# Kernel tuning notes

Measured on AMD Instinct MI355X. Metric: run time of the kernel, lower is better.

Reference implementation:

```python
import jax, jax.numpy as jnp
import numpy as np

U, I, D = 100000, 100000, 64
B, T = 16384, 1_638_400
R = 5  # rating levels 1..5


def setup_inputs() -> dict:
    key = jax.random.key(0)
    ks = jax.random.split(key, 8)
    return {
        "user_idx": jax.random.randint(ks[0], (B,), 0, U, dtype=jnp.int32),
        "item_idx": jax.random.randint(ks[1], (B,), 0, I, dtype=jnp.int32),
        "flat_items": jax.random.randint(ks[2], (T,), 0, I, dtype=jnp.int32),
        "seg_ids": jnp.sort(jax.random.randint(ks[3], (T,), 0, B * R, dtype=jnp.int32)),
        "user_emb": (jax.random.uniform(ks[4], (U, D), dtype=jnp.float32) - 0.5) * 0.01,
        "item_emb": (jax.random.uniform(ks[5], (I, D), dtype=jnp.float32) - 0.5) * 0.01,
        "Mr": (jax.random.uniform(ks[6], (I, D), dtype=jnp.float32) - 0.5) * 0.01,
        "user_bias": jnp.zeros((U,), dtype=jnp.float32),
        "item_bias": jnp.zeros((I,), dtype=jnp.float32),
        "global_avg": jnp.float32(3.5),
    }


def reference(user_idx, item_idx, flat_items, seg_ids, user_emb, item_emb, Mr, user_bias, item_bias, global_avg):
    num_seg = B * R  # segment = sample_i * 5 + (rating - 1)
    # Original torch code does Mr_ik(rate_dict).sum() -> scalar over ALL dims,
    # then broadcasts that scalar onto the latent_dim vector UuMpc[i].
    row_sum = Mr[flat_items].sum(axis=-1)  # [T] per-item full-row sum
    # Emulate `rate_dict.remove(item_idx[i])`: mask out the target item of this sample.
    match = flat_items == item_idx[seg_ids // R]  # [T]
    contrib = jnp.where(match, 0.0, row_sum)
    seg_sum = jax.ops.segment_sum(contrib, seg_ids, num_segments=num_seg)  # [B*5]
    cnt = jax.ops.segment_sum(jnp.where(match, 0.0, 1.0), seg_ids, num_segments=num_seg)
    per_seg = jnp.where(cnt > 0, seg_sum / jnp.sqrt(jnp.maximum(cnt, 1.0)), 0.0)
    uu_mpc = per_seg.reshape(B, R).sum(axis=-1)  # [B] scalar per sample
    user_vec = user_emb[user_idx] + uu_mpc[:, None]  # broadcast scalar over latent dim
    item_vec = item_emb[item_idx]
    rui = (user_vec * item_vec).sum(axis=-1) + user_bias[user_idx] + item_bias[item_idx] + global_avg
    return jnp.clip(rui, 1.0, 5.0)
```

## Files before the change

### kernel.cpp

```cpp
#include <hip/hip_runtime.h>

#define U_N 100000
#define I_N 100000
#define D_N 64
#define B_N 16384
#define T_N 1638400
#define R_N 5
#define NSEG (B_N * R_N)

#define RS_THREADS (I_N * 16)
#define BD_THREADS (T_N / 4)
#define K1_THREADS (RS_THREADS + BD_THREADS)

__global__ void prep_kernel(const float* __restrict__ Mr,
                            const int* __restrict__ seg_ids,
                            float* __restrict__ rowsum,
                            int* __restrict__ seg_start) {
    int gtid = blockIdx.x * blockDim.x + threadIdx.x;
    if (gtid < RS_THREADS) {
        int row = gtid >> 4;
        int sub = gtid & 15;
        const float4* p = (const float4*)(Mr + (long)row * D_N);
        float4 v4 = p[sub];
        float v = v4.x + v4.y + v4.z + v4.w;
        v += __shfl_xor(v, 1);
        v += __shfl_xor(v, 2);
        v += __shfl_xor(v, 4);
        v += __shfl_xor(v, 8);
        if (sub == 0) rowsum[row] = v;
    } else {
        int t4 = gtid - RS_THREADS;
        if (t4 >= BD_THREADS) return;
        int base = t4 * 4;
        int4 s4 = ((const int4*)seg_ids)[t4];
        int sv0 = (base == 0) ? -1 : seg_ids[base - 1];
        int sv1 = s4.x, sv2 = s4.y, sv3 = s4.z, sv4 = s4.w;
        for (int s = sv0 + 1; s <= sv1; ++s) seg_start[s] = base + 0;
        for (int s = sv1 + 1; s <= sv2; ++s) seg_start[s] = base + 1;
        for (int s = sv2 + 1; s <= sv3; ++s) seg_start[s] = base + 2;
        for (int s = sv3 + 1; s <= sv4; ++s) seg_start[s] = base + 3;
        if (base + 4 == T_N) {
            for (int s = sv4 + 1; s <= NSEG; ++s) seg_start[s] = T_N;
        }
    }
}

__device__ __forceinline__ void count_matches(unsigned long long m, int tb,
                                              int e0, int e1, int e2, int e3,
                                              int e4, int e5, int* mcnt) {
    if (m) {
        int ea[6] = {e0, e1, e2, e3, e4, e5};
        #pragma unroll
        for (int r = 0; r < 5; ++r) {
            int a = ea[r] - tb;     a = a < 0 ? 0 : (a > 64 ? 64 : a);
            int bb = ea[r + 1] - tb; bb = bb < 0 ? 0 : (bb > 64 ? 64 : bb);
            if (bb > a) {
                unsigned long long hiM = (bb == 64) ? ~0ULL : ((1ULL << bb) - 1ULL);
                unsigned long long loM = (1ULL << a) - 1ULL;
                mcnt[r] += __popcll(m & hiM & ~loM);
            }
        }
    }
}

__global__ void sample_kernel(const int* __restrict__ user_idx,
                              const int* __restrict__ item_idx,
                              const int* __restrict__ flat_items,
                              const float* __restrict__ user_emb,
                              const float* __restrict__ item_emb,
                              const float* __restrict__ user_bias,
                              const float* __restrict__ item_bias,
                              const float* __restrict__ global_avg,
                              const float* __restrict__ rowsum,
                              const int* __restrict__ seg_start,
                              float* __restrict__ out) {
    int lane = threadIdx.x & 63;
    int b    = (blockIdx.x * blockDim.x + threadIdx.x) >> 6;
    if (b >= B_N) return;

    int u      = user_idx[b];
    int target = item_idx[b];
    float ue = user_emb[(long)u * D_N + lane];
    float ie = item_emb[(long)target * D_N + lane];

    int e0 = seg_start[b * R_N + 0];
    int e1 = seg_start[b * R_N + 1];
    int e2 = seg_start[b * R_N + 2];
    int e3 = seg_start[b * R_N + 3];
    int e4 = seg_start[b * R_N + 4];
    int e5 = seg_start[b * R_N + 5];
    int lo = e0, hi = e5;

    int t0 = lo + lane, t1 = lo + 64 + lane;
    bool ok0 = t0 < hi, ok1 = t1 < hi;
    int fi0 = -1, fi1 = -1;
    float rv0 = 0.f, rv1 = 0.f;
    if (ok0) fi0 = flat_items[t0];
    if (ok1) fi1 = flat_items[t1];
    if (ok0) rv0 = rowsum[fi0];
    if (ok1) rv1 = rowsum[fi1];

    int mcnt[5] = {0, 0, 0, 0, 0};
    unsigned long long m0 = __ballot(ok0 && fi0 == target);
    unsigned long long m1 = __ballot(ok1 && fi1 == target);
    count_matches(m0, lo,      e0, e1, e2, e3, e4, e5, mcnt);
    count_matches(m1, lo + 64, e0, e1, e2, e3, e4, e5, mcnt);
    for (int tb = lo + 128; tb < hi; tb += 64) {
        int t = tb + lane;
        bool ok = t < hi;
        int fi = ok ? flat_items[t] : -1;
        unsigned long long m = __ballot(ok && fi == target);
        count_matches(m, tb, e0, e1, e2, e3, e4, e5, mcnt);
    }

    int c0 = (e1 - e0) - mcnt[0];
    int c1 = (e2 - e1) - mcnt[1];
    int c2 = (e3 - e2) - mcnt[2];
    int c3 = (e4 - e3) - mcnt[3];
    int c4 = (e5 - e4) - mcnt[4];
    float w0 = c0 > 0 ? rsqrtf((float)c0) : 0.f;
    float w1 = c1 > 0 ? rsqrtf((float)c1) : 0.f;
    float w2 = c2 > 0 ? rsqrtf((float)c2) : 0.f;
    float w3 = c3 > 0 ? rsqrtf((float)c3) : 0.f;
    float w4 = c4 > 0 ? rsqrtf((float)c4) : 0.f;

    float acc = 0.f;
    if (ok0 && fi0 != target) {
        float w = t0 >= e1 ? (t0 >= e2 ? (t0 >= e3 ? (t0 >= e4 ? w4 : w3) : w2) : w1) : w0;
        acc += rv0 * w;
    }
    if (ok1 && fi1 != target) {
        float w = t1 >= e1 ? (t1 >= e2 ? (t1 >= e3 ? (t1 >= e4 ? w4 : w3) : w2) : w1) : w0;
        acc += rv1 * w;
    }
    for (int tb = lo + 128; tb < hi; tb += 64) {
        int t = tb + lane;
        if (t < hi) {
            int fi = flat_items[t];
            if (fi != target) {
                float rv = rowsum[fi];
                float w = t >= e1 ? (t >= e2 ? (t >= e3 ? (t >= e4 ? w4 : w3) : w2) : w1) : w0;
                acc += rv * w;
            }
        }
    }

    float dot = ue * ie;
    float isum = ie;
    #pragma unroll
    for (int off = 32; off >= 1; off >>= 1) {
        acc  += __shfl_xor(acc, off);
        dot  += __shfl_xor(dot, off);
        isum += __shfl_xor(isum, off);
    }
    if (lane == 0) {
        float rui = dot + acc * isum + user_bias[u] + item_bias[target] + global_avg[0];
        rui = fminf(fmaxf(rui, 1.0f), 5.0f);
        out[b] = rui;
    }
}

extern "C" void kernel_launch(void* const* d_in, const int* in_sizes, int n_in,
                              void* d_out, int out_size, void* d_ws, size_t ws_size,
                              hipStream_t stream) {
    const int*   user_idx   = (const int*)d_in[0];
    const int*   item_idx   = (const int*)d_in[1];
    const int*   flat_items = (const int*)d_in[2];
    const int*   seg_ids    = (const int*)d_in[3];
    const float* user_emb   = (const float*)d_in[4];
    const float* item_emb   = (const float*)d_in[5];
    const float* Mr         = (const float*)d_in[6];
    const float* user_bias  = (const float*)d_in[7];
    const float* item_bias  = (const float*)d_in[8];
    const float* global_avg = (const float*)d_in[9];
    float* out = (float*)d_out;

    float* rowsum    = (float*)d_ws;
    int*   seg_start = (int*)(rowsum + I_N);

    prep_kernel<<<(K1_THREADS + 255) / 256, 256, 0, stream>>>(
        Mr, seg_ids, rowsum, seg_start);
    sample_kernel<<<B_N / 4, 256, 0, stream>>>(
        user_idx, item_idx, flat_items, user_emb, item_emb,
        user_bias, item_bias, global_avg, rowsum, seg_start, out);
}
```

Baseline: 136.8 us.

## Move embedding dot products into prep kernel and vectorize first segment chunk

The user/item embedding gathers, dot product, item-sum and bias terms move from the sample kernel into extra threads of the prep kernel, which stores a float2 per sample. The sample kernel then handles only the rating-history scan. Its first 256 entries are loaded as one int4 per lane, with per-rating match counts computed by ballots, and later tiles use a simpler ballot-based rating bucket. The intent is to take the embedding latency off the scan kernel and overlap it with the row-sum work. The cost is a larger prep kernel and an extra workspace round trip.

Result: slower. 140.9 us (+3.0%).

```diff
diff --git a/kernel.cpp b/kernel.cpp
--- a/kernel.cpp
+++ b/kernel.cpp
@@ -10,12 +10,21 @@
 
 #define RS_THREADS (I_N * 16)
 #define BD_THREADS (T_N / 4)
-#define K1_THREADS (RS_THREADS + BD_THREADS)
+#define DOT_THREADS (B_N * 64)
+#define K1_THREADS (RS_THREADS + BD_THREADS + DOT_THREADS)
 
 __global__ void prep_kernel(const float* __restrict__ Mr,
                             const int* __restrict__ seg_ids,
+                            const int* __restrict__ user_idx,
+                            const int* __restrict__ item_idx,
+                            const float* __restrict__ user_emb,
+                            const float* __restrict__ item_emb,
+                            const float* __restrict__ user_bias,
+                            const float* __restrict__ item_bias,
+                            const float* __restrict__ global_avg,
                             float* __restrict__ rowsum,
-                            int* __restrict__ seg_start) {
+                            int* __restrict__ seg_start,
+                            float2* __restrict__ pre_isum) {
     int gtid = blockIdx.x * blockDim.x + threadIdx.x;
     if (gtid < RS_THREADS) {
         int row = gtid >> 4;
@@ -28,9 +37,8 @@
         v += __shfl_xor(v, 4);
         v += __shfl_xor(v, 8);
         if (sub == 0) rowsum[row] = v;
-    } else {
+    } else if (gtid < RS_THREADS + BD_THREADS) {
         int t4 = gtid - RS_THREADS;
-        if (t4 >= BD_THREADS) return;
         int base = t4 * 4;
         int4 s4 = ((const int4*)seg_ids)[t4];
         int sv0 = (base == 0) ? -1 : seg_ids[base - 1];
@@ -42,46 +50,45 @@
         if (base + 4 == T_N) {
             for (int s = sv4 + 1; s <= NSEG; ++s) seg_start[s] = T_N;
         }
+    } else {
+        int gt2  = gtid - (RS_THREADS + BD_THREADS);
+        int b    = gt2 >> 6;
+        int lane = gt2 & 63;
+        int u      = user_idx[b];
+        int target = item_idx[b];
+        float ue = user_emb[(long)u * D_N + lane];
+        float ie = item_emb[(long)target * D_N + lane];
+        float ub = user_bias[u];
+        float ib = item_bias[target];
+        float g  = global_avg[0];
+        float dot = ue * ie;
+        float isum = ie;
+        #pragma unroll
+        for (int off = 32; off >= 1; off >>= 1) {
+            dot  += __shfl_xor(dot, off);
+            isum += __shfl_xor(isum, off);
+        }
+        if (lane == 0) {
+            float2 r;
+            r.x = dot + ub + ib + g;
+            r.y = isum;
+            pre_isum[b] = r;
+        }
     }
 }
 
-__device__ __forceinline__ void count_matches(unsigned long long m, int tb,
-                                              int e0, int e1, int e2, int e3,
-                                              int e4, int e5, int* mcnt) {
-    if (m) {
-        int ea[6] = {e0, e1, e2, e3, e4, e5};
-        #pragma unroll
-        for (int r = 0; r < 5; ++r) {
-            int a = ea[r] - tb;     a = a < 0 ? 0 : (a > 64 ? 64 : a);
-            int bb = ea[r + 1] - tb; bb = bb < 0 ? 0 : (bb > 64 ? 64 : bb);
-            if (bb > a) {
-                unsigned long long hiM = (bb == 64) ? ~0ULL : ((1ULL << bb) - 1ULL);
-                unsigned long long loM = (1ULL << a) - 1ULL;
-                mcnt[r] += __popcll(m & hiM & ~loM);
-            }
-        }
-    }
-}
-
-__global__ void sample_kernel(const int* __restrict__ user_idx,
-                              const int* __restrict__ item_idx,
+__global__ void sample_kernel(const int* __restrict__ item_idx,
                               const int* __restrict__ flat_items,
-                              const float* __restrict__ user_emb,
-                              const float* __restrict__ item_emb,
-                              const float* __restrict__ user_bias,
-                              const float* __restrict__ item_bias,
-                              const float* __restrict__ global_avg,
                               const float* __restrict__ rowsum,
                               const int* __restrict__ seg_start,
+                              const float2* __restrict__ pre_isum,
                               float* __restrict__ out) {
     int lane = threadIdx.x & 63;
     int b    = (blockIdx.x * blockDim.x + threadIdx.x) >> 6;
     if (b >= B_N) return;
 
-    int u      = user_idx[b];
     int target = item_idx[b];
-    float ue = user_emb[(long)u * D_N + lane];
-    float ie = item_emb[(long)target * D_N + lane];
+    float2 pi  = pre_isum[b];
 
     int e0 = seg_start[b * R_N + 0];
     int e1 = seg_start[b * R_N + 1];
@@ -91,26 +98,50 @@
     int e5 = seg_start[b * R_N + 5];
     int lo = e0, hi = e5;
 
-    int t0 = lo + lane, t1 = lo + 64 + lane;
-    bool ok0 = t0 < hi, ok1 = t1 < hi;
-    int fi0 = -1, fi1 = -1;
-    float rv0 = 0.f, rv1 = 0.f;
-    if (ok0) fi0 = flat_items[t0];
-    if (ok1) fi1 = flat_items[t1];
-    if (ok0) rv0 = rowsum[fi0];
-    if (ok1) rv1 = rowsum[fi1];
-
-    int mcnt[5] = {0, 0, 0, 0, 0};
-    unsigned long long m0 = __ballot(ok0 && fi0 == target);
-    unsigned long long m1 = __ballot(ok1 && fi1 == target);
-    count_matches(m0, lo,      e0, e1, e2, e3, e4, e5, mcnt);
-    count_matches(m1, lo + 64, e0, e1, e2, e3, e4, e5, mcnt);
-    for (int tb = lo + 128; tb < hi; tb += 64) {
+    int base = lo & ~3;
+    int t0 = base + 4 * lane;
+
+    int4 fi4 = make_int4(-1, -1, -1, -1);
+    if (t0 < hi) fi4 = ((const int4*)(flat_items + base))[lane];
+    int  fi[4] = {fi4.x, fi4.y, fi4.z, fi4.w};
+    bool ok[4], mt[4];
+    int  rj[4];
+    float rv[4] = {0.f, 0.f, 0.f, 0.f};
+    #pragma unroll
+    for (int j = 0; j < 4; ++j) {
+        int t = t0 + j;
+        ok[j] = (t >= lo) & (t < hi);
+        rj[j] = (t >= e1) + (t >= e2) + (t >= e3) + (t >= e4);
+        mt[j] = ok[j] && (fi[j] == target);
+    }
+    #pragma unroll
+    for (int j = 0; j < 4; ++j) {
+        if (ok[j]) rv[j] = rowsum[fi[j]];
+    }
+
+    int mcnt[R_N] = {0, 0, 0, 0, 0};
+    unsigned long long anym = __ballot(mt[0] | mt[1] | mt[2] | mt[3]);
+    if (anym) {
+        #pragma unroll
+        for (int j = 0; j < 4; ++j) {
+            #pragma unroll
+            for (int r = 0; r < R_N; ++r) {
+                mcnt[r] += __popcll(__ballot(mt[j] && rj[j] == r));
+            }
+        }
+    }
+    for (int tb = base + 256; tb < hi; tb += 64) {
         int t = tb + lane;
-        bool ok = t < hi;
-        int fi = ok ? flat_items[t] : -1;
-        unsigned long long m = __ballot(ok && fi == target);
-        count_matches(m, tb, e0, e1, e2, e3, e4, e5, mcnt);
+        bool okt = t < hi;
+        int f = okt ? flat_items[t] : -1;
+        unsigned long long m = __ballot(okt && f == target);
+        if (m) {
+            int r = (t >= e1) + (t >= e2) + (t >= e3) + (t >= e4);
+            #pragma unroll
+            for (int rr = 0; rr < R_N; ++rr) {
+                mcnt[rr] += __popcll(m & __ballot(r == rr));
+            }
+        }
     }
 
     int c0 = (e1 - e0) - mcnt[0];
@@ -125,36 +156,31 @@
     float w4 = c4 > 0 ? rsqrtf((float)c4) : 0.f;
 
     float acc = 0.f;
-    if (ok0 && fi0 != target) {
-        float w = t0 >= e1 ? (t0 >= e2 ? (t0 >= e3 ? (t0 >= e4 ? w4 : w3) : w2) : w1) : w0;
-        acc += rv0 * w;
-    }
-    if (ok1 && fi1 != target) {
-        float w = t1 >= e1 ? (t1 >= e2 ? (t1 >= e3 ? (t1 >= e4 ? w4 : w3) : w2) : w1) : w0;
-        acc += rv1 * w;
-    }
-    for (int tb = lo + 128; tb < hi; tb += 64) {
+    #pragma unroll
+    for (int j = 0; j < 4; ++j) {
+        if (ok[j] && !mt[j]) {
+            int r = rj[j];
+            float w = r == 0 ? w0 : (r == 1 ? w1 : (r == 2 ? w2 : (r == 3 ? w3 : w4)));
+            acc += rv[j] * w;
+        }
+    }
+    for (int tb = base + 256; tb < hi; tb += 64) {
         int t = tb + lane;
         if (t < hi) {
-            int fi = flat_items[t];
-            if (fi != target) {
-                float rv = rowsum[fi];
-                float w = t >= e1 ? (t >= e2 ? (t >= e3 ? (t >= e4 ? w4 : w3) : w2) : w1) : w0;
-                acc += rv * w;
+            int f = flat_items[t];
+            if (f != target) {
+                int r = (t >= e1) + (t >= e2) + (t >= e3) + (t >= e4);
+                float w = r == 0 ? w0 : (r == 1 ? w1 : (r == 2 ? w2 : (r == 3 ? w3 : w4)));
+                acc += rowsum[f] * w;
             }
         }
     }
 
-    float dot = ue * ie;
-    float isum = ie;
-    #pragma unroll
-    for (int off = 32; off >= 1; off >>= 1) {
-        acc  += __shfl_xor(acc, off);
-        dot  += __shfl_xor(dot, off);
-        isum += __shfl_xor(isum, off);
-    }
+    #pragma unroll
+    for (int off = 32; off >= 1; off >>= 1) acc += __shfl_xor(acc, off);
+
     if (lane == 0) {
-        float rui = dot + acc * isum + user_bias[u] + item_bias[target] + global_avg[0];
+        float rui = pi.x + acc * pi.y;
         rui = fminf(fmaxf(rui, 1.0f), 5.0f);
         out[b] = rui;
     }
@@ -175,12 +201,13 @@
     const float* global_avg = (const float*)d_in[9];
     float* out = (float*)d_out;
 
-    float* rowsum    = (float*)d_ws;
-    int*   seg_start = (int*)(rowsum + I_N);
-
-    prep_kernel<<<(K1_THREADS + 255) / 256, 256, 0, stream>>>(
-        Mr, seg_ids, rowsum, seg_start);
+    float*  rowsum    = (float*)d_ws;
+    int*    seg_start = (int*)((char*)d_ws + 400000);
+    float2* pre_isum  = (float2*)((char*)d_ws + 400000 + 327696);
+
+    prep_kernel<<<K1_THREADS / 256, 256, 0, stream>>>(
+        Mr, seg_ids, user_idx, item_idx, user_emb, item_emb,
+        user_bias, item_bias, global_avg, rowsum, seg_start, pre_isum);
     sample_kernel<<<B_N / 4, 256, 0, stream>>>(
-        user_idx, item_idx, flat_items, user_emb, item_emb,
-        user_bias, item_bias, global_avg, rowsum, seg_start, out);
+        item_idx, flat_items, rowsum, seg_start, pre_isum, out);
 }
```
